# Kernel tuning notes

Measured on AMD Instinct MI355X. Metric: run time of the kernel, lower is better.

## Reference

```python
import jax, jax.numpy as jnp
import numpy as np

B, L, D = 8, 1024, 768
H, W, Dd = 16, 16, 4          # token grid, H*W*Dd == L
N, R, K = 16, 48, 4           # d_state, dt_rank, d_conv
EPS = 1e-5


def _physical_pos_embed(batch_params, has_velocity):
    # physical coords [B, L, 3]: (distance, angle, velocity/time)
    h_idx = jnp.arange(H, dtype=jnp.float32)[None, :, None, None]
    w_idx = jnp.arange(W, dtype=jnp.float32)[None, None, :, None]
    d_idx = jnp.arange(Dd, dtype=jnp.float32)[None, None, None, :]
    rres = batch_params[:, 0][:, None, None, None]
    ares = batch_params[:, 1][:, None, None, None]
    vres = batch_params[:, 2][:, None, None, None]
    zero = jnp.zeros((1, H, W, Dd), jnp.float32)
    dist = h_idx * rres + zero
    ang = (w_idx - W / 2) * ares + zero
    vel = jnp.where(has_velocity[:, None, None, None],
                    (d_idx - Dd / 2) * vres, d_idx * vres) + zero
    coords = jnp.stack([dist, ang, vel], axis=-1).reshape(B, L, 3)
    mx = coords.max(axis=1, keepdims=True)
    mn = coords.min(axis=1, keepdims=True)
    rng = mx - mn
    rng = jnp.where(rng > 0, rng, jnp.ones_like(rng))
    coords = (coords - mn) / rng
    # sincos embed: D/3 = 256 dims per coord (even -> pure sin/cos)
    fdim = D // 3
    omega = jnp.arange(fdim // 2, dtype=jnp.float32) / (fdim / 2.0)
    omega = 1.0 / (10000.0 ** omega)                      # [128]
    out = jnp.einsum('blc,f->blcf', coords, omega)        # [B,L,3,128]
    emb = jnp.concatenate([jnp.sin(out), jnp.cos(out)], axis=-1)  # [B,L,3,256]
    return emb.reshape(B, L, D)


def _rmsnorm(x, w):
    return x * jax.lax.rsqrt(jnp.mean(x * x, axis=-1, keepdims=True) + EPS) * w


def _mamba(h, in_proj_w, in_proj_b, conv_w, conv_b, x_proj_w,
           dt_proj_w, dt_proj_b, A_log, D_param, out_proj_w, out_proj_b):
    xz = h @ in_proj_w.T + in_proj_b                      # [B,L,2D]
    x_in, z = xz[..., :D], xz[..., D:]
    # causal depthwise conv1d, kernel K
    xp = jnp.pad(x_in, ((0, 0), (K - 1, 0), (0, 0)))
    x_conv = sum(xp[:, k:k + L, :] * conv_w[:, 0, k] for k in range(K))
    x_conv = jax.nn.silu(x_conv + conv_b)
    x_dbl = x_conv @ x_proj_w.T                           # [B,L,R+2N]
    dt, Bm, Cm = x_dbl[..., :R], x_dbl[..., R:R + N], x_dbl[..., R + N:]
    dt = jax.nn.softplus(dt @ dt_proj_w.T + dt_proj_b)    # [B,L,D]
    A = -jnp.exp(A_log)                                   # [D,N]
    dA = jnp.exp(dt[..., None] * A)                       # [B,L,D,N]
    dBx = dt[..., None] * Bm[:, :, None, :] * x_conv[..., None]

    def step(hst, inp):
        dA_t, dBx_t, C_t = inp
        hst = dA_t * hst + dBx_t                          # [B,D,N]
        y_t = jnp.einsum('bdn,bn->bd', hst, C_t)
        return hst, y_t

    h0 = jnp.zeros((B, D, N), x_in.dtype)
    _, ys = jax.lax.scan(step, h0, (dA.transpose(1, 0, 2, 3),
                                    dBx.transpose(1, 0, 2, 3),
                                    Cm.transpose(1, 0, 2)))
    y = ys.transpose(1, 0, 2) + D_param * x_conv          # [B,L,D]
    y = y * jax.nn.silu(z)
    return y @ out_proj_w.T + out_proj_b


def reference(x, batch_params, has_velocity, norm_w, in_proj_w, in_proj_b,
              conv_w, conv_b, x_proj_w, dt_proj_w, dt_proj_b, A_log,
              D_param, out_proj_w, out_proj_b):
    pos = _physical_pos_embed(batch_params, has_velocity)
    residual = x + pos                                    # ARBlock residual
    hidden = _rmsnorm(residual, norm_w)
    hidden = _mamba(hidden, in_proj_w, in_proj_b, conv_w, conv_b, x_proj_w,
                    dt_proj_w, dt_proj_b, A_log, D_param,
                    out_proj_w, out_proj_b)
    return hidden + residual


def setup_inputs():
    key = jax.random.key(0)
    ks = jax.random.split(key, 12)
    s = 0.02
    return {
        'x': jax.random.normal(ks[0], (B, L, D), jnp.float32),
        'batch_params': jax.random.uniform(ks[1], (B, 4), jnp.float32, 0.01, 1.0),
        'has_velocity': jax.random.randint(ks[2], (B,), 0, 2) > 0,
        'norm_w': jnp.ones((D,), jnp.float32),
        'in_proj_w': jax.random.normal(ks[3], (2 * D, D), jnp.float32) * s,
        'in_proj_b': jnp.zeros((2 * D,), jnp.float32),
        'conv_w': jax.random.normal(ks[4], (D, 1, K), jnp.float32) * 0.3,
        'conv_b': jnp.zeros((D,), jnp.float32),
        'x_proj_w': jax.random.normal(ks[5], (R + 2 * N, D), jnp.float32) * s,
        'dt_proj_w': jax.random.normal(ks[6], (D, R), jnp.float32) * s,
        'dt_proj_b': jax.random.normal(ks[7], (D,), jnp.float32) * 0.1,
        'A_log': jnp.log(jax.random.uniform(ks[8], (D, N), jnp.float32, 1.0, 16.0)),
        'D_param': jnp.ones((D,), jnp.float32),
        'out_proj_w': jax.random.normal(ks[9], (D, D), jnp.float32) * s,
        'out_proj_b': jnp.zeros((D,), jnp.float32),
    }
```

## Files before the change

### kernel.cpp

```cpp
#include <hip/hip_runtime.h>
#include <math.h>

#define BB 8
#define LL 1024
#define DD 768
#define NNs 16
#define RR 48

typedef __attribute__((ext_vector_type(8))) short bf16x8;
typedef __attribute__((ext_vector_type(4))) float f32x4;
typedef __attribute__((ext_vector_type(2))) float f32x2;

__device__ __forceinline__ float silu_f(float v) { return v / (1.0f + __expf(-v)); }

__device__ __forceinline__ short f2bf(float f) {
    union { float f; unsigned u; } v; v.f = f;
    unsigned r = (v.u + 0x7fffu + ((v.u >> 16) & 1u)) >> 16;
    return (short)r;
}

__device__ __forceinline__ float exp2_fast(float x) {
    float r;
    asm("v_exp_f32 %0, %1" : "=v"(r) : "v"(x));
    return r;
}

__device__ __forceinline__ f32x2 pk_fma(f32x2 a, f32x2 b, f32x2 c) {
    f32x2 d;
    asm("v_pk_fma_f32 %0, %1, %2, %3" : "=v"(d) : "v"(a), "v"(b), "v"(c));
    return d;
}
__device__ __forceinline__ f32x2 pk_mul(f32x2 a, f32x2 b) {
    f32x2 d;
    asm("v_pk_mul_f32 %0, %1, %2" : "=v"(d) : "v"(a), "v"(b));
    return d;
}

__device__ __forceinline__ void async16(const void* g, void* l) {
    __builtin_amdgcn_global_load_lds((const __attribute__((address_space(1))) void*)g,
                                     (__attribute__((address_space(3))) void*)l,
                                     16, 0, 0);
}

__global__ __launch_bounds__(256) void k_cvt2(const float* __restrict__ s1,
                                              short* __restrict__ d1, int n1,
                                              const float* __restrict__ s2,
                                              short* __restrict__ d2, int n2) {
    int i = blockIdx.x * 256 + threadIdx.x;
    if (i < n1) {
        float4 v = ((const float4*)s1)[i];
        short4 o = { f2bf(v.x), f2bf(v.y), f2bf(v.z), f2bf(v.w) };
        ((short4*)d1)[i] = o;
    } else {
        int j = i - n1;
        if (j < n2) {
            float4 v = ((const float4*)s2)[j];
            short4 o = { f2bf(v.x), f2bf(v.y), f2bf(v.z), f2bf(v.w) };
            ((short4*)d2)[j] = o;
        }
    }
}

__global__ __launch_bounds__(256) void k_pos_rms(const float* __restrict__ x,
                                                 const float* __restrict__ norm_w,
                                                 float* __restrict__ res,
                                                 short* __restrict__ hidb) {
    int row = blockIdx.x;
    int l = row & (LL - 1);
    int d3 = l & 3;
    int w = (l >> 2) & 15;
    int h = l >> 6;
    float coord[3] = { h * (1.0f / 15.0f), w * (1.0f / 15.0f), d3 * (1.0f / 3.0f) };
    const float LOG1E4 = 9.210340371976184f;
    int t = threadIdx.x;
    float r[3];
    float s = 0.0f;
#pragma unroll
    for (int i = 0; i < 3; i++) {
        int j = t + i * 256;
        int c = j >> 8;
        int fp = j & 255;
        int f = fp & 127;
        float omega = __expf(-(f * (1.0f / 128.0f)) * LOG1E4);
        float arg = coord[c] * omega;
        float pv = (fp < 128) ? __sinf(arg) : __cosf(arg);
        float rv = x[(size_t)row * DD + j] + pv;
        r[i] = rv;
        s += rv * rv;
    }
#pragma unroll
    for (int off = 32; off; off >>= 1) s += __shfl_xor(s, off, 64);
    __shared__ float ls[4];
    if ((t & 63) == 0) ls[t >> 6] = s;
    __syncthreads();
    s = ls[0] + ls[1] + ls[2] + ls[3];
    float rs = rsqrtf(s * (1.0f / DD) + 1e-5f);
#pragma unroll
    for (int i = 0; i < 3; i++) {
        int j = t + i * 256;
        res[(size_t)row * DD + j] = r[i];
        hidb[(size_t)row * DD + j] = f2bf(r[i] * rs * norm_w[j]);
    }
}

template <int EPI, bool AF32>
__global__ __launch_bounds__(256) void gemm_mfma(const void* __restrict__ Ap,
                                                 const short* __restrict__ Bw,
                                                 int Kd,
                                                 const float* __restrict__ bias,
                                                 const float* __restrict__ resid,
                                                 float* __restrict__ C0,
                                                 float* __restrict__ C1) {
    __shared__ short As[4096];
    __shared__ short Bs[4096];
    int m0 = blockIdx.y * 128;
    int n0 = blockIdx.x * 128;
    int tid = threadIdx.x;
    int lane = tid & 63, wave = tid >> 6;
    int q = lane >> 4, r = lane & 15;
    int wm = wave >> 1, wn = wave & 1;

    const size_t Kb = (size_t)Kd * 2;
    const char* gB0 = (const char*)Bw + (size_t)(n0 + wave * 16 + r) * Kb + q * 16;
    const char* gB1 = gB0 + 64 * Kb;
    char* lB0 = (char*)Bs + wave * 1024;
    char* lB1 = lB0 + 4096;
    const char* gA0 = nullptr; const char* gA1 = nullptr;
    char* lA0 = nullptr; char* lA1 = nullptr;
    if (!AF32) {
        gA0 = (const char*)Ap + (size_t)(m0 + wave * 16 + r) * Kb + q * 16;
        gA1 = gA0 + 64 * Kb;
        lA0 = (char*)As + wave * 1024;
        lA1 = lA0 + 4096;
    }

    f32x4 acc[4][4] = {};

    for (int k0 = 0; k0 < Kd; k0 += 32) {
        if (AF32) {
            const float* Af = (const float*)Ap;
#pragma unroll
            for (int p = 0; p < 2; p++) {
                int m = m0 + (p * 4 + wave) * 16 + r;
                const float* src = Af + (size_t)m * Kd + k0 + q * 8;
                float4 v0 = *(const float4*)src;
                float4 v1 = *(const float4*)(src + 4);
                bf16x8 pk;
                pk[0] = f2bf(v0.x); pk[1] = f2bf(v0.y);
                pk[2] = f2bf(v0.z); pk[3] = f2bf(v0.w);
                pk[4] = f2bf(v1.x); pk[5] = f2bf(v1.y);
                pk[6] = f2bf(v1.z); pk[7] = f2bf(v1.w);
                *(bf16x8*)&As[p * 2048 + wave * 512 + lane * 8] = pk;
            }
        } else {
            async16(gA0, lA0); async16(gA1, lA1);
            gA0 += 64; gA1 += 64;
        }
        async16(gB0, lB0); async16(gB1, lB1);
        gB0 += 64; gB1 += 64;
        __syncthreads();
        bf16x8 af[4], bf[4];
#pragma unroll
        for (int a = 0; a < 4; a++)
            af[a] = *(const bf16x8*)&As[((wm * 4 + a) * 64 + q * 16 + r) * 8];
#pragma unroll
        for (int b = 0; b < 4; b++)
            bf[b] = *(const bf16x8*)&Bs[((wn * 4 + b) * 64 + q * 16 + r) * 8];
#pragma unroll
        for (int a = 0; a < 4; a++)
#pragma unroll
            for (int b = 0; b < 4; b++)
                acc[a][b] = __builtin_amdgcn_mfma_f32_16x16x32_bf16(
                    af[a], bf[b], acc[a][b], 0, 0, 0);
        __syncthreads();
    }

#pragma unroll
    for (int a = 0; a < 4; a++) {
        int mrow = m0 + (wm * 4 + a) * 16 + q * 4;
#pragma unroll
        for (int b = 0; b < 4; b++) {
            int ncol = n0 + (wn * 4 + b) * 16 + r;
            float bb = bias[ncol];
            if (EPI == 1) {
                float* dst = (ncol < DD) ? (C0 + (size_t)mrow * DD + ncol)
                                         : (C1 + (size_t)mrow * DD + (ncol - DD));
#pragma unroll
                for (int e = 0; e < 4; e++)
                    dst[(size_t)e * DD] = acc[a][b][e] + bb;
            } else {
#pragma unroll
                for (int e = 0; e < 4; e++) {
                    size_t idx = (size_t)(mrow + e) * DD + ncol;
                    C0[idx] = acc[a][b][e] + bb + resid[idx];
                }
            }
        }
    }
}

__global__ __launch_bounds__(256) void k_xproj(const float* __restrict__ A,
                                               const float* __restrict__ Bw,
                                               float* __restrict__ part) {
    __shared__ __align__(16) float As[16][68];
    __shared__ __align__(16) float Bs[16][84];
    int kbase = blockIdx.x * 96;
    int m0 = blockIdx.y * 64;
    int t = threadIdx.x;
    int tx = t & 15, ty = t >> 4;
    int ar = t >> 2;
    int ak = (t & 3) * 4;
    float acc[4][5] = {};
    for (int k0 = kbase; k0 < kbase + 96; k0 += 16) {
        float4 av = *(const float4*)(A + (size_t)(m0 + ar) * DD + k0 + ak);
        As[ak + 0][ar] = av.x; As[ak + 1][ar] = av.y;
        As[ak + 2][ar] = av.z; As[ak + 3][ar] = av.w;
        for (int idx = t; idx < 320; idx += 256) {
            int row = idx >> 2, kq = (idx & 3) * 4;
            float4 bv = *(const float4*)(Bw + (size_t)row * DD + k0 + kq);
            Bs[kq + 0][row] = bv.x; Bs[kq + 1][row] = bv.y;
            Bs[kq + 2][row] = bv.z; Bs[kq + 3][row] = bv.w;
        }
        __syncthreads();
#pragma unroll
        for (int kk = 0; kk < 16; kk++) {
            float4 a4 = *(const float4*)&As[kk][ty * 4];
            float aa[4] = { a4.x, a4.y, a4.z, a4.w };
            float b0 = Bs[kk][tx * 5 + 0];
            float b1 = Bs[kk][tx * 5 + 1];
            float b2 = Bs[kk][tx * 5 + 2];
            float b3 = Bs[kk][tx * 5 + 3];
            float b4 = Bs[kk][tx * 5 + 4];
#pragma unroll
            for (int i = 0; i < 4; i++) {
                acc[i][0] += aa[i] * b0; acc[i][1] += aa[i] * b1;
                acc[i][2] += aa[i] * b2; acc[i][3] += aa[i] * b3;
                acc[i][4] += aa[i] * b4;
            }
        }
        __syncthreads();
    }
    float* dst = part + (size_t)blockIdx.x * (BB * LL * 80);
#pragma unroll
    for (int i = 0; i < 4; i++) {
        int m = m0 + ty * 4 + i;
#pragma unroll
        for (int j = 0; j < 5; j++)
            dst[(size_t)m * 80 + tx * 5 + j] = acc[i][j];
    }
}

__global__ __launch_bounds__(256) void k_xred(const float* __restrict__ part,
                                              float* __restrict__ xdbl) {
    const size_t n4 = (size_t)BB * LL * 80 / 4;
    size_t i = (size_t)blockIdx.x * 256 + threadIdx.x;
    if (i >= n4) return;
    const float4* p4 = (const float4*)part;
    float4 s = p4[i];
#pragma unroll
    for (int c = 1; c < 8; c++) {
        float4 v = p4[c * n4 + i];
        s.x += v.x; s.y += v.y; s.z += v.z; s.w += v.w;
    }
    ((float4*)xdbl)[i] = s;
}

template <int MODE>
__global__ __launch_bounds__(256) void gemm_nt(const float* __restrict__ A, int lda,
                                               const float* __restrict__ Bw, int ldb,
                                               int N, int Kd,
                                               const float* __restrict__ bias,
                                               float* __restrict__ C0, int ldc) {
    __shared__ __align__(16) float As[16][68];
    __shared__ __align__(16) float Bs[16][68];
    int m0 = blockIdx.y * 64;
    int n0 = blockIdx.x * 64;
    int t = threadIdx.x;
    int tx = t & 15, ty = t >> 4;
    int ar = t >> 2;
    int ak = (t & 3) * 4;
    float acc[4][4] = {};
    for (int k0 = 0; k0 < Kd; k0 += 16) {
        float4 av = *(const float4*)(A + (size_t)(m0 + ar) * lda + k0 + ak);
        int brow = n0 + ar;
        if (brow >= N) brow = N - 1;
        float4 bv = *(const float4*)(Bw + (size_t)brow * ldb + k0 + ak);
        As[ak + 0][ar] = av.x; As[ak + 1][ar] = av.y;
        As[ak + 2][ar] = av.z; As[ak + 3][ar] = av.w;
        Bs[ak + 0][ar] = bv.x; Bs[ak + 1][ar] = bv.y;
        Bs[ak + 2][ar] = bv.z; Bs[ak + 3][ar] = bv.w;
        __syncthreads();
#pragma unroll
        for (int kk = 0; kk < 16; kk++) {
            float4 a4 = *(const float4*)&As[kk][ty * 4];
            float4 b4 = *(const float4*)&Bs[kk][tx * 4];
            float aa[4] = { a4.x, a4.y, a4.z, a4.w };
            float bb[4] = { b4.x, b4.y, b4.z, b4.w };
#pragma unroll
            for (int i = 0; i < 4; i++)
#pragma unroll
                for (int j = 0; j < 4; j++) acc[i][j] += aa[i] * bb[j];
        }
        __syncthreads();
    }
    if (MODE == 0) {
#pragma unroll
        for (int i = 0; i < 4; i++) {
            int m = m0 + ty * 4 + i;
#pragma unroll
            for (int j = 0; j < 4; j++) {
                int n = n0 + tx * 4 + j;
                if (n < N) C0[(size_t)m * ldc + n] = acc[i][j];
            }
        }
    } else {
        float4 bi = *(const float4*)(bias + n0 + tx * 4);
        float bl[4] = { bi.x, bi.y, bi.z, bi.w };
#pragma unroll
        for (int i = 0; i < 4; i++) {
            int m = m0 + ty * 4 + i;
            float v[4];
#pragma unroll
            for (int j = 0; j < 4; j++) {
                float u = acc[i][j] + bl[j];
                v[j] = (u > 20.0f) ? u : log1pf(__expf(u));
            }
            float4 o = { v[0], v[1], v[2], v[3] };
            *(float4*)(C0 + (size_t)m * DD + n0 + tx * 4) = o;
        }
    }
}

__global__ __launch_bounds__(256) void k_conv(const float* __restrict__ xin,
                                              const float* __restrict__ cw,
                                              const float* __restrict__ cb,
                                              float* __restrict__ xc) {
    size_t g4 = (size_t)blockIdx.x * 256 + threadIdx.x;
    int d = (int)((g4 * 4) % DD);
    int bt = (int)(g4 * 4 / DD);
    int tt = bt & (LL - 1);
    const float* p = xin + (size_t)bt * DD + d;
    float4 zr = { 0.f, 0.f, 0.f, 0.f };
    float4 x0 = (tt >= 3) ? *(const float4*)(p - 3 * DD) : zr;
    float4 x1 = (tt >= 2) ? *(const float4*)(p - 2 * DD) : zr;
    float4 x2 = (tt >= 1) ? *(const float4*)(p - 1 * DD) : zr;
    float4 x3 = *(const float4*)p;
    const float4* cw4 = (const float4*)cw;
    float4 w0 = cw4[d + 0], w1 = cw4[d + 1], w2 = cw4[d + 2], w3 = cw4[d + 3];
    float4 cbv = *(const float4*)(cb + d);
    float4 o;
    o.x = silu_f(cbv.x + x0.x * w0.x + x1.x * w0.y + x2.x * w0.z + x3.x * w0.w);
    o.y = silu_f(cbv.y + x0.y * w1.x + x1.y * w1.y + x2.y * w1.z + x3.y * w1.w);
    o.z = silu_f(cbv.z + x0.z * w2.x + x1.z * w2.y + x2.z * w2.z + x3.z * w2.w);
    o.w = silu_f(cbv.w + x0.w * w3.x + x1.w * w3.y + x2.w * w3.z + x3.w * w3.w);
    *(float4*)(xc + g4 * 4) = o;
}

template <bool YB>
__global__ __launch_bounds__(256, 3) void k_scan(const float* __restrict__ dtf,
                                                 const float* __restrict__ xc,
                                                 const float* __restrict__ xdbl,
                                                 const float* __restrict__ A_log,
                                                 const float* __restrict__ Dp,
                                                 float* __restrict__ zy,
                                                 short* __restrict__ yb) {
    __shared__ float Pl[32 * 8 * 16];
    __shared__ float Sl[32 * 8 * 16];
    int bid = blockIdx.x;
    int xcd = bid & 7;
    int v = bid >> 3;
    int dtile = xcd * 12 + (v % 12);
    int b = v / 12;
    int d0 = dtile * 8;
    int tid = threadIdx.x;
    int dl = tid & 7;
    int c = tid >> 3;
    int d = d0 + dl;

    const float LOG2E = 1.4426950408889634f;
    f32x2 Ac2[8];
    {
        const float4* al = (const float4*)(A_log + d * NNs);
#pragma unroll
        for (int i = 0; i < 4; i++) {
            float4 v4 = al[i];
            Ac2[i * 2]     = (f32x2){ -__expf(v4.x) * LOG2E, -__expf(v4.y) * LOG2E };
            Ac2[i * 2 + 1] = (f32x2){ -__expf(v4.z) * LOG2E, -__expf(v4.w) * LOG2E };
        }
    }
    size_t rb = ((size_t)(b * LL + c * 32)) * DD + d;
    const float* dtp = dtf + rb;
    const float* xcp = xc + rb;
    float* zp = zy + rb;
    short* ybp = yb + rb;
    const float* xrow = xdbl + ((size_t)(b * LL + c * 32)) * 80 + RR;

    f32x2 S2[8];
#pragma unroll
    for (int k = 0; k < 8; k++) S2[k] = (f32x2){ 0.0f, 0.0f };
    float dtsum = 0.0f;
    {
        float dt0 = dtp[0], xc0 = xcp[0];
        float dt1 = dtp[DD], xc1 = xcp[DD];
        float4 Bb[4];
#pragma unroll
        for (int qq = 0; qq < 4; qq++) Bb[qq] = *(const float4*)(xrow + qq * 4);
        for (int i = 0; i < 32; i++) {
            int i2 = (i + 2 < 32) ? i + 2 : 31;
            int i1 = (i + 1 < 32) ? i + 1 : 31;
            float dt2 = dtp[(size_t)i2 * DD];
            float xc2 = xcp[(size_t)i2 * DD];
            float4 nB[4];
            const float* nBr = xrow + i1 * 80;
#pragma unroll
            for (int qq = 0; qq < 4; qq++) nB[qq] = *(const float4*)(nBr + qq * 4);

            float dx = dt0 * xc0;
            dtsum += dt0;
            f32x2 dtp2 = (f32x2){ dt0, dt0 };
            f32x2 dx2 = (f32x2){ dx, dx };
#pragma unroll
            for (int k = 0; k < 8; k++) {
                float4 qb = Bb[k >> 1];
                f32x2 bl2 = (k & 1) ? (f32x2){ qb.z, qb.w } : (f32x2){ qb.x, qb.y };
                f32x2 arg = pk_mul(dtp2, Ac2[k]);
                f32x2 e2;
                e2[0] = exp2_fast(arg[0]);
                e2[1] = exp2_fast(arg[1]);
                f32x2 dxb = pk_mul(dx2, bl2);
                S2[k] = pk_fma(e2, S2[k], dxb);
            }
            dt0 = dt1; dt1 = dt2;
            xc0 = xc1; xc1 = xc2;
#pragma unroll
            for (int qq = 0; qq < 4; qq++) Bb[qq] = nB[qq];
        }
    }
    {
        float* pw = &Pl[(c * 8 + dl) * 16];
        float* sw = &Sl[(c * 8 + dl) * 16];
#pragma unroll
        for (int q2 = 0; q2 < 4; q2++) {
            float4 pv = { exp2_fast(Ac2[q2 * 2][0] * dtsum),
                          exp2_fast(Ac2[q2 * 2][1] * dtsum),
                          exp2_fast(Ac2[q2 * 2 + 1][0] * dtsum),
                          exp2_fast(Ac2[q2 * 2 + 1][1] * dtsum) };
            float4 sv = { S2[q2 * 2][0], S2[q2 * 2][1],
                          S2[q2 * 2 + 1][0], S2[q2 * 2 + 1][1] };
            *(float4*)(pw + q2 * 4) = pv;
            *(float4*)(sw + q2 * 4) = sv;
        }
    }
    __syncthreads();
    if (tid < 128) {
        int d2 = tid >> 4, n2 = tid & 15;
        float hh = 0.0f;
#pragma unroll
        for (int cc = 0; cc < 32; cc++) {
            int idx = (cc * 8 + d2) * 16 + n2;
            float Pv = Pl[idx], Sv = Sl[idx];
            Pl[idx] = hh;
            hh = Pv * hh + Sv;
        }
    }
    __syncthreads();
    f32x2 h2[8];
    {
        const float* hr = &Pl[(c * 8 + dl) * 16];
#pragma unroll
        for (int q2 = 0; q2 < 4; q2++) {
            float4 v4 = *(const float4*)(hr + q2 * 4);
            h2[q2 * 2]     = (f32x2){ v4.x, v4.y };
            h2[q2 * 2 + 1] = (f32x2){ v4.z, v4.w };
        }
    }
    float Dv = Dp[d];
    {
        float dt0 = dtp[0], xc0 = xcp[0], zv0 = zp[0];
        float dt1 = dtp[DD], xc1 = xcp[DD], zv1 = zp[DD];
        float4 Bb[4], Cc[4];
#pragma unroll
        for (int qq = 0; qq < 4; qq++) {
            Bb[qq] = *(const float4*)(xrow + qq * 4);
            Cc[qq] = *(const float4*)(xrow + 16 + qq * 4);
        }
        for (int i = 0; i < 32; i++) {
            int i2 = (i + 2 < 32) ? i + 2 : 31;
            int i1 = (i + 1 < 32) ? i + 1 : 31;
            float dt2 = dtp[(size_t)i2 * DD];
            float xc2 = xcp[(size_t)i2 * DD];
            float zv2 = zp[(size_t)i2 * DD];
            float4 nB[4], nC[4];
            const float* nBr = xrow + i1 * 80;
#pragma unroll
            for (int qq = 0; qq < 4; qq++) {
                nB[qq] = *(const float4*)(nBr + qq * 4);
                nC[qq] = *(const float4*)(nBr + 16 + qq * 4);
            }
            float dx = dt0 * xc0;
            f32x2 dtp2 = (f32x2){ dt0, dt0 };
            f32x2 dx2 = (f32x2){ dx, dx };
            f32x2 y2 = (f32x2){ Dv * xc0, 0.0f };
#pragma unroll
            for (int k = 0; k < 8; k++) {
                float4 qb = Bb[k >> 1];
                float4 qc = Cc[k >> 1];
                f32x2 bl2 = (k & 1) ? (f32x2){ qb.z, qb.w } : (f32x2){ qb.x, qb.y };
                f32x2 cl2 = (k & 1) ? (f32x2){ qc.z, qc.w } : (f32x2){ qc.x, qc.y };
                f32x2 arg = pk_mul(dtp2, Ac2[k]);
                f32x2 e2;
                e2[0] = exp2_fast(arg[0]);
                e2[1] = exp2_fast(arg[1]);
                f32x2 dxb = pk_mul(dx2, bl2);
                h2[k] = pk_fma(e2, h2[k], dxb);
                y2 = pk_fma(h2[k], cl2, y2);
            }
            float y = y2[0] + y2[1];
            float gated = y * silu_f(zv0);
            if (YB) ybp[(size_t)i * DD] = f2bf(gated);
            else    zp[(size_t)i * DD] = gated;
            dt0 = dt1; dt1 = dt2;
            xc0 = xc1; xc1 = xc2;
            zv0 = zv1; zv1 = zv2;
#pragma unroll
            for (int qq = 0; qq < 4; qq++) { Bb[qq] = nB[qq]; Cc[qq] = nC[qq]; }
        }
    }
}

extern "C" void kernel_launch(void* const* d_in, const int* in_sizes, int n_in,
                              void* d_out, int out_size, void* d_ws, size_t ws_size,
                              hipStream_t stream) {
    const float* x      = (const float*)d_in[0];
    const float* norm_w = (const float*)d_in[3];
    const float* in_w   = (const float*)d_in[4];
    const float* in_b   = (const float*)d_in[5];
    const float* conv_w = (const float*)d_in[6];
    const float* conv_b = (const float*)d_in[7];
    const float* xp_w   = (const float*)d_in[8];
    const float* dt_w   = (const float*)d_in[9];
    const float* dt_b   = (const float*)d_in[10];
    const float* A_log  = (const float*)d_in[11];
    const float* Dp     = (const float*)d_in[12];
    const float* out_w  = (const float*)d_in[13];
    const float* out_b  = (const float*)d_in[14];
    float* out = (float*)d_out;

    const size_t S = (size_t)BB * LL * DD;
    const size_t X = (size_t)BB * LL * 80;
    float* res   = (float*)d_ws;
    float* slotA = res + S;
    float* slotB = slotA + S;
    float* zf    = slotB + S;
    float* xdbl  = zf + S;
    short* inw_b  = (short*)(xdbl + X);
    short* outw_b = inw_b + 1536 * DD;
    short* ybf    = outw_b + DD * DD;
    float* xpart  = (float*)(ybf + S);

    short* hidb = (short*)slotA;
    float* xc   = slotA;
    float* xin  = slotB;
    float* dtf  = slotB;

    const int M = BB * LL;

    size_t needYB = (size_t)((char*)(ybf + S) - (char*)d_ws);
    size_t needXP = (size_t)((char*)(xpart + 8 * X) - (char*)d_ws);
    bool useYB = ws_size >= needYB;
    bool useXP = ws_size >= needXP;

    {
        int n1 = 1536 * DD / 4, n2 = DD * DD / 4;
        k_cvt2<<<(n1 + n2 + 255) / 256, 256, 0, stream>>>(in_w, inw_b, n1,
                                                          out_w, outw_b, n2);
    }

    k_pos_rms<<<M, 256, 0, stream>>>(x, norm_w, res, hidb);

    gemm_mfma<1, false><<<dim3(1536 / 128, M / 128), 256, 0, stream>>>(
        hidb, inw_b, DD, in_b, nullptr, xin, zf);

    k_conv<<<(int)(S / 1024), 256, 0, stream>>>(xin, conv_w, conv_b, xc);

    if (useXP) {
        k_xproj<<<dim3(8, M / 64), 256, 0, stream>>>(xc, xp_w, xpart);
        k_xred<<<(int)(X / 4 + 255) / 256, 256, 0, stream>>>(xpart, xdbl);
    } else {
        gemm_nt<0><<<dim3(2, M / 64), 256, 0, stream>>>(
            xc, DD, xp_w, DD, RR + 2 * NNs, DD, nullptr, xdbl, 80);
    }

    gemm_nt<2><<<dim3(DD / 64, M / 64), 256, 0, stream>>>(
        xdbl, 80, dt_w, RR, DD, RR, dt_b, dtf, DD);

    if (useYB) {
        k_scan<true><<<768, 256, 0, stream>>>(dtf, xc, xdbl, A_log, Dp, zf, ybf);
        gemm_mfma<3, false><<<dim3(DD / 128, M / 128), 256, 0, stream>>>(
            ybf, outw_b, DD, out_b, res, out, nullptr);
    } else {
        k_scan<false><<<768, 256, 0, stream>>>(dtf, xc, xdbl, A_log, Dp, zf, ybf);
        gemm_mfma<3, true><<<dim3(DD / 128, M / 128), 256, 0, stream>>>(
            zf, outw_b, DD, out_b, res, out, nullptr);
    }
}
```

Measured before the change: 336.0 us.

## Use 128x64-tile MFMA out-projection GEMM and deepen scan prefetch distance

Adds a new out-projection GEMM kernel with 128x64 tiles, so the 768-wide output gets twice as many blocks (12x64 instead of 6x64) for better CU occupancy on the final GEMM. Separately, the scan kernel's per-timestep loads of dt, xc and z are now prefetched four steps ahead instead of two, to hide global memory latency. The smaller N tile lowers data reuse per block, and the deeper prefetch adds register pressure.

Result: no change. 330.9 us (-1.5%).

```diff
diff --git a/kernel.cpp b/kernel.cpp
--- a/kernel.cpp
+++ b/kernel.cpp
@@ -194,6 +194,90 @@
                     size_t idx = (size_t)(mrow + e) * DD + ncol;
                     C0[idx] = acc[a][b][e] + bb + resid[idx];
                 }
+            }
+        }
+    }
+}
+
+template <bool AF32>
+__global__ __launch_bounds__(256) void gemm_mfma_n64(const void* __restrict__ Ap,
+                                                     const short* __restrict__ Bw,
+                                                     int Kd,
+                                                     const float* __restrict__ bias,
+                                                     const float* __restrict__ resid,
+                                                     float* __restrict__ C0) {
+    __shared__ short As[4096];
+    __shared__ short Bs[2048];
+    int m0 = blockIdx.y * 128;
+    int n0 = blockIdx.x * 64;
+    int tid = threadIdx.x;
+    int lane = tid & 63, wave = tid >> 6;
+    int q = lane >> 4, r = lane & 15;
+
+    const size_t Kb = (size_t)Kd * 2;
+    const char* gB0 = (const char*)Bw + (size_t)(n0 + wave * 16 + r) * Kb + q * 16;
+    char* lB0 = (char*)Bs + wave * 1024;
+    const char* gA0 = nullptr; const char* gA1 = nullptr;
+    char* lA0 = nullptr; char* lA1 = nullptr;
+    if (!AF32) {
+        gA0 = (const char*)Ap + (size_t)(m0 + wave * 16 + r) * Kb + q * 16;
+        gA1 = gA0 + 64 * Kb;
+        lA0 = (char*)As + wave * 1024;
+        lA1 = lA0 + 4096;
+    }
+
+    f32x4 acc[2][4] = {};
+
+    for (int k0 = 0; k0 < Kd; k0 += 32) {
+        if (AF32) {
+            const float* Af = (const float*)Ap;
+#pragma unroll
+            for (int p = 0; p < 2; p++) {
+                int m = m0 + (p * 4 + wave) * 16 + r;
+                const float* src = Af + (size_t)m * Kd + k0 + q * 8;
+                float4 v0 = *(const float4*)src;
+                float4 v1 = *(const float4*)(src + 4);
+                bf16x8 pk;
+                pk[0] = f2bf(v0.x); pk[1] = f2bf(v0.y);
+                pk[2] = f2bf(v0.z); pk[3] = f2bf(v0.w);
+                pk[4] = f2bf(v1.x); pk[5] = f2bf(v1.y);
+                pk[6] = f2bf(v1.z); pk[7] = f2bf(v1.w);
+                *(bf16x8*)&As[p * 2048 + wave * 512 + lane * 8] = pk;
+            }
+        } else {
+            async16(gA0, lA0); async16(gA1, lA1);
+            gA0 += 64; gA1 += 64;
+        }
+        async16(gB0, lB0);
+        gB0 += 64;
+        __syncthreads();
+        bf16x8 af[2], bf[4];
+#pragma unroll
+        for (int a = 0; a < 2; a++)
+            af[a] = *(const bf16x8*)&As[((wave * 2 + a) * 64 + q * 16 + r) * 8];
+#pragma unroll
+        for (int b = 0; b < 4; b++)
+            bf[b] = *(const bf16x8*)&Bs[(b * 64 + q * 16 + r) * 8];
+#pragma unroll
+        for (int a = 0; a < 2; a++)
+#pragma unroll
+            for (int b = 0; b < 4; b++)
+                acc[a][b] = __builtin_amdgcn_mfma_f32_16x16x32_bf16(
+                    af[a], bf[b], acc[a][b], 0, 0, 0);
+        __syncthreads();
+    }
+
+#pragma unroll
+    for (int a = 0; a < 2; a++) {
+        int mrow = m0 + (wave * 2 + a) * 16 + q * 4;
+#pragma unroll
+        for (int b = 0; b < 4; b++) {
+            int ncol = n0 + b * 16 + r;
+            float bb = bias[ncol];
+#pragma unroll
+            for (int e = 0; e < 4; e++) {
+                size_t idx = (size_t)(mrow + e) * DD + ncol;
+                C0[idx] = acc[a][b][e] + bb + resid[idx];
             }
         }
     }
@@ -400,16 +484,18 @@
     for (int k = 0; k < 8; k++) S2[k] = (f32x2){ 0.0f, 0.0f };
     float dtsum = 0.0f;
     {
-        float dt0 = dtp[0], xc0 = xcp[0];
-        float dt1 = dtp[DD], xc1 = xcp[DD];
+        float dt0 = dtp[0],      xc0 = xcp[0];
+        float dt1 = dtp[DD],     xc1 = xcp[DD];
+        float dt2 = dtp[2 * DD], xc2 = xcp[2 * DD];
+        float dt3 = dtp[3 * DD], xc3 = xcp[3 * DD];
         float4 Bb[4];
 #pragma unroll
         for (int qq = 0; qq < 4; qq++) Bb[qq] = *(const float4*)(xrow + qq * 4);
         for (int i = 0; i < 32; i++) {
-            int i2 = (i + 2 < 32) ? i + 2 : 31;
+            int i4 = (i + 4 < 32) ? i + 4 : 31;
             int i1 = (i + 1 < 32) ? i + 1 : 31;
-            float dt2 = dtp[(size_t)i2 * DD];
-            float xc2 = xcp[(size_t)i2 * DD];
+            float dtn = dtp[(size_t)i4 * DD];
+            float xcn = xcp[(size_t)i4 * DD];
             float4 nB[4];
             const float* nBr = xrow + i1 * 80;
 #pragma unroll
@@ -430,8 +516,8 @@
                 f32x2 dxb = pk_mul(dx2, bl2);
                 S2[k] = pk_fma(e2, S2[k], dxb);
             }
-            dt0 = dt1; dt1 = dt2;
-            xc0 = xc1; xc1 = xc2;
+            dt0 = dt1; dt1 = dt2; dt2 = dt3; dt3 = dtn;
+            xc0 = xc1; xc1 = xc2; xc2 = xc3; xc3 = xcn;
 #pragma unroll
             for (int qq = 0; qq < 4; qq++) Bb[qq] = nB[qq];
         }
@@ -476,8 +562,10 @@
     }
     float Dv = Dp[d];
     {
-        float dt0 = dtp[0], xc0 = xcp[0], zv0 = zp[0];
-        float dt1 = dtp[DD], xc1 = xcp[DD], zv1 = zp[DD];
+        float dt0 = dtp[0],      xc0 = xcp[0],      zv0 = zp[0];
+        float dt1 = dtp[DD],     xc1 = xcp[DD],     zv1 = zp[DD];
+        float dt2 = dtp[2 * DD], xc2 = xcp[2 * DD], zv2 = zp[2 * DD];
+        float dt3 = dtp[3 * DD], xc3 = xcp[3 * DD], zv3 = zp[3 * DD];
         float4 Bb[4], Cc[4];
 #pragma unroll
         for (int qq = 0; qq < 4; qq++) {
@@ -485,11 +573,11 @@
             Cc[qq] = *(const float4*)(xrow + 16 + qq * 4);
         }
         for (int i = 0; i < 32; i++) {
-            int i2 = (i + 2 < 32) ? i + 2 : 31;
+            int i4 = (i + 4 < 32) ? i + 4 : 31;
             int i1 = (i + 1 < 32) ? i + 1 : 31;
-            float dt2 = dtp[(size_t)i2 * DD];
-            float xc2 = xcp[(size_t)i2 * DD];
-            float zv2 = zp[(size_t)i2 * DD];
+            float dtn = dtp[(size_t)i4 * DD];
+            float xcn = xcp[(size_t)i4 * DD];
+            float zvn = zp[(size_t)i4 * DD];
             float4 nB[4], nC[4];
             const float* nBr = xrow + i1 * 80;
 #pragma unroll
@@ -519,9 +607,9 @@
             float gated = y * silu_f(zv0);
             if (YB) ybp[(size_t)i * DD] = f2bf(gated);
             else    zp[(size_t)i * DD] = gated;
-            dt0 = dt1; dt1 = dt2;
-            xc0 = xc1; xc1 = xc2;
-            zv0 = zv1; zv1 = zv2;
+            dt0 = dt1; dt1 = dt2; dt2 = dt3; dt3 = dtn;
+            xc0 = xc1; xc1 = xc2; xc2 = xc3; xc3 = xcn;
+            zv0 = zv1; zv1 = zv2; zv2 = zv3; zv3 = zvn;
 #pragma unroll
             for (int qq = 0; qq < 4; qq++) { Bb[qq] = nB[qq]; Cc[qq] = nC[qq]; }
         }
@@ -596,11 +684,11 @@
 
     if (useYB) {
         k_scan<true><<<768, 256, 0, stream>>>(dtf, xc, xdbl, A_log, Dp, zf, ybf);
-        gemm_mfma<3, false><<<dim3(DD / 128, M / 128), 256, 0, stream>>>(
-            ybf, outw_b, DD, out_b, res, out, nullptr);
+        gemm_mfma_n64<false><<<dim3(DD / 64, M / 128), 256, 0, stream>>>(
+            ybf, outw_b, DD, out_b, res, out);
     } else {
         k_scan<false><<<768, 256, 0, stream>>>(dtf, xc, xdbl, A_log, Dp, zf, ybf);
-        gemm_mfma<3, true><<<dim3(DD / 128, M / 128), 256, 0, stream>>>(
-            zf, outw_b, DD, out_b, res, out, nullptr);
-    }
-}
+        gemm_mfma_n64<true><<<dim3(DD / 64, M / 128), 256, 0, stream>>>(
+            zf, outw_b, DD, out_b, res, out);
+    }
+}
```
